# Performance work log

Hardware: AMD Instinct MI355X
Metric: run time of the kernel (lower is better)

The kernel has to match this reference:

```python
import jax, jax.numpy as jnp
import numpy as np

N = 100000        # nodes
E = 3200000       # edges (avg degree 32)
D_IN, D_H, D_OUT = 128, 128, 64
EPS = 1e-5        # BatchNorm eps


def setup_inputs() -> dict:
    key = jax.random.key(0)
    ks = jax.random.split(key, 12)
    s = 0.1
    return {
        "x": jax.random.normal(ks[0], (N, D_IN), jnp.float32),
        "edge_index": jax.random.randint(ks[1], (2, E), 0, N, jnp.int32),
        "W1": jax.random.normal(ks[2], (D_IN, D_H), jnp.float32) * s,
        "b1": jnp.zeros((D_H,), jnp.float32),
        "W2": jax.random.normal(ks[3], (D_H, D_H), jnp.float32) * s,
        "b2": jnp.zeros((D_H,), jnp.float32),
        "W3": jax.random.normal(ks[4], (D_H, D_OUT), jnp.float32) * s,
        "b3": jnp.zeros((D_OUT,), jnp.float32),
        "g1": jnp.ones((D_H,), jnp.float32),
        "be1": jnp.zeros((D_H,), jnp.float32),
        "g2": jnp.ones((D_H,), jnp.float32),
        "be2": jnp.zeros((D_H,), jnp.float32),
    }


def reference(x, edge_index, W1, b1, W2, b2, W3, b3, g1, be1, g2, be2):
    # GCNConv normalization: add self-loops, symmetric deg^-1/2 A deg^-1/2
    loop = jnp.arange(N, dtype=edge_index.dtype)
    src = jnp.concatenate([edge_index[0], loop])   # [E+N]
    dst = jnp.concatenate([edge_index[1], loop])   # [E+N]
    deg = jax.ops.segment_sum(jnp.ones(src.shape, x.dtype), dst, num_segments=N)
    dinv = jnp.where(deg > 0, jax.lax.rsqrt(deg), 0.0)
    norm = (dinv[src] * dinv[dst])[:, None]        # [E+N, 1]

    def conv(h, W, b):
        h = h @ W                                   # dense transform [N, d]
        msg = h[src] * norm                         # gather + scale [E+N, d]
        return jax.ops.segment_sum(msg, dst, num_segments=N) + b

    def bn(h, g, be):  # BatchNorm1d over nodes (batch stats, eval-style dropout)
        m = h.mean(axis=0)
        v = h.var(axis=0)
        return (h - m) * jax.lax.rsqrt(v + EPS) * g + be

    h = jax.nn.relu(bn(conv(x, W1, b1), g1, be1))
    h = jax.nn.relu(bn(conv(h, W2, b2), g2, be2))
    h = conv(h, W3, b3)
    return jax.nn.softmax(h, axis=1)
```

## Files before the change

### kernel.cpp

```cpp
#include <hip/hip_runtime.h>
#include <hip/hip_fp16.h>

constexpr int   NN   = 100000;
constexpr int   NE   = 3200000;
constexpr float BN_EPS = 1e-5f;

constexpr int MG_B  = (NN / 32 + 3) / 4;
constexpr int NB    = (NN + 127) / 128;
constexpr int HB    = 256;
constexpr int CHUNK = NE / HB;
constexpr int BKT_CAP = 5120;
constexpr int IDX_CAP = 1536;
constexpr int NPAN = 8;

typedef _Float16 half8 __attribute__((ext_vector_type(8)));
typedef float    floatx16 __attribute__((ext_vector_type(16)));
typedef float    floatx8  __attribute__((ext_vector_type(8)));
typedef int      intx4   __attribute__((ext_vector_type(4)));


__global__ __launch_bounds__(256) void k_wprep_all(const float* __restrict__ W1,
                                                   const float* __restrict__ W2,
                                                   const float* __restrict__ W3,
                                                   _Float16* __restrict__ Wt1,
                                                   _Float16* __restrict__ Wt2,
                                                   _Float16* __restrict__ Wt3) {
  int idx = blockIdx.x * 256 + threadIdx.x;
  if (idx < 16384) {
    int k = idx >> 7, n = idx & 127;
    Wt1[n * 128 + k] = (_Float16)W1[idx];
  } else if (idx < 32768) {
    int j = idx - 16384, k = j >> 7, n = j & 127;
    Wt2[n * 128 + k] = (_Float16)W2[j];
  } else if (idx < 40960) {
    int j = idx - 32768, k = j >> 6, n = j & 63;
    Wt3[n * 128 + k] = (_Float16)W3[j];
  }
}

__global__ __launch_bounds__(256) void k_f1(const int* __restrict__ dst,
                                            int* __restrict__ blkhist,
                                            const float* __restrict__ x,
                                            const _Float16* __restrict__ Wt1,
                                            _Float16* __restrict__ C) {
  __shared__ int h[NB];
  if (blockIdx.x < MG_B) {
    int wid  = (blockIdx.x * 256 + threadIdx.x) >> 6;
    int lane = threadIdx.x & 63;
    if (wid >= NN / 32) return;
    const int m = lane & 31;
    const int q = lane >> 5;
    const int row0 = wid * 32;
    const float* Arow = x + (size_t)(row0 + m) * 128 + q * 8;

    floatx16 acc[4] = {};
#pragma unroll
    for (int s = 0; s < 8; ++s) {
      float4 a0 = *(const float4*)(Arow + 16 * s);
      float4 a1 = *(const float4*)(Arow + 16 * s + 4);
      half8 af;
      af[0] = (_Float16)a0.x; af[1] = (_Float16)a0.y;
      af[2] = (_Float16)a0.z; af[3] = (_Float16)a0.w;
      af[4] = (_Float16)a1.x; af[5] = (_Float16)a1.y;
      af[6] = (_Float16)a1.z; af[7] = (_Float16)a1.w;
#pragma unroll
      for (int ct = 0; ct < 4; ++ct) {
        half8 bf = *(const half8*)(Wt1 + (size_t)(ct * 32 + m) * 128 + q * 8 + 16 * s);
        acc[ct] = __builtin_amdgcn_mfma_f32_32x32x16_f16(af, bf, acc[ct], 0, 0, 0);
      }
    }
#pragma unroll
    for (int ct = 0; ct < 4; ++ct) {
      int p = ct * 2 + (m >> 4);
      int off = m & 15;
#pragma unroll
      for (int r = 0; r < 16; ++r) {
        int row = (r & 3) + 8 * (r >> 2) + 4 * q;
        C[((size_t)p * NN + row0 + row) * 16 + off] = (_Float16)acc[ct][r];
      }
    }
  } else {
    int j = blockIdx.x - MG_B;
    int t = threadIdx.x;
    for (int b = t; b < NB; b += 256) h[b] = 0;
    __syncthreads();
    int base = j * CHUNK;
    for (int e = base + t; e < base + CHUNK; e += 256)
      atomicAdd(&h[dst[e] >> 7], 1);
    __syncthreads();
    for (int b = t; b < NB; b += 256) blkhist[j * NB + b] = h[b];
  }
}

__global__ __launch_bounds__(256) void k_scan_bkt_a(const int* __restrict__ blkhist,
                                                    int* __restrict__ blkbase,
                                                    int* __restrict__ total) {
  int wid  = (blockIdx.x * 256 + threadIdx.x) >> 6;
  int lane = threadIdx.x & 63;
  if (wid >= NB) return;
  int i0 = lane * 4;
  int v0 = blkhist[(i0 + 0) * NB + wid];
  int v1 = blkhist[(i0 + 1) * NB + wid];
  int v2 = blkhist[(i0 + 2) * NB + wid];
  int v3 = blkhist[(i0 + 3) * NB + wid];
  int lt = v0 + v1 + v2 + v3;
  int inc = lt;
#pragma unroll
  for (int off = 1; off < 64; off <<= 1) {
    int xx = __shfl_up(inc, off);
    if (lane >= off) inc += xx;
  }
  int exc = inc - lt;
  blkbase[(i0 + 0) * NB + wid] = exc;
  blkbase[(i0 + 1) * NB + wid] = exc + v0;
  blkbase[(i0 + 2) * NB + wid] = exc + v0 + v1;
  blkbase[(i0 + 3) * NB + wid] = exc + v0 + v1 + v2;
  if (lane == 63) total[wid] = inc;
}

__global__ __launch_bounds__(1024) void k_scan_bkt_b(const int* __restrict__ total,
                                                     int* __restrict__ bbase) {
  __shared__ int s[1024];
  int t = threadIdx.x;
  int v = (t < NB) ? total[t] : 0;
  s[t] = v;
  __syncthreads();
  for (int off = 1; off < 1024; off <<= 1) {
    int xx = (t >= off) ? s[t - off] : 0;
    __syncthreads();
    s[t] += xx;
    __syncthreads();
  }
  if (t < NB) bbase[t] = s[t] - v;
  if (t == NB - 1) bbase[NB] = s[t];
}

__global__ __launch_bounds__(256) void k_scatter(const int* __restrict__ ei,
                                                 const int* __restrict__ bbase,
                                                 const int* __restrict__ blkbase,
                                                 int* __restrict__ ebuf) {
  __shared__ int cur[NB];
  int i = blockIdx.x;
  int t = threadIdx.x;
  for (int b = t; b < NB; b += 256) cur[b] = bbase[b] + blkbase[i * NB + b];
  __syncthreads();
  int base = i * CHUNK;
  for (int e = base + t; e < base + CHUNK; e += 256) {
    int s = ei[e];
    int d = ei[NE + e];
    int b = d >> 7;
    int pos = atomicAdd(&cur[b], 1);
    ebuf[pos] = s | ((d & 127) << 17);
  }
}

__global__ __launch_bounds__(256) void k_bucket(const int* __restrict__ bbase,
                                                const int* __restrict__ ebuf,
                                                int* __restrict__ rowptr,
                                                float* __restrict__ dinv,
                                                int* __restrict__ csrc,
                                                _Float16* __restrict__ Hf) {
  __shared__ int degL[128];
  __shared__ int sc[128];
  __shared__ int curL[128];
  __shared__ float dvs[128];
  __shared__ int sorted[BKT_CAP];
  int b = blockIdx.x;
  int t = threadIdx.x;
  int e0 = bbase[b], e1 = bbase[b + 1];
  int cnt = e1 - e0;
  if (t < 128) degL[t] = 0;
  __syncthreads();
  for (int e = e0 + t; e < e1; e += 256)
    atomicAdd(&degL[ebuf[e] >> 17], 1);
  __syncthreads();
  if (t < 128) sc[t] = degL[t];
  __syncthreads();
  for (int off = 1; off < 128; off <<= 1) {
    int xx = 0;
    if (t < 128 && t >= off) xx = sc[t - off];
    __syncthreads();
    if (t < 128) sc[t] += xx;
    __syncthreads();
  }
  if (t < 128) {
    int node = b * 128 + t;
    float dv = 0.f;
    if (node < NN) {
      int d = degL[t];
      int exc = sc[t] - d;
      rowptr[node] = e0 + exc;
      dv = rsqrtf((float)(d + 1));
      dinv[node] = dv;
      curL[t] = exc;
    }
    dvs[t] = dv;
  }
  if (b == NB - 1 && t == 0) rowptr[NN] = NE;
  __syncthreads();
  if (cnt <= BKT_CAP) {
    for (int e = e0 + t; e < e1; e += 256) {
      int p = ebuf[e];
      int pos = atomicAdd(&curL[p >> 17], 1);
      sorted[pos] = p & 0x1FFFF;
    }
    __syncthreads();
    for (int i = t; i < cnt; i += 256) csrc[e0 + i] = sorted[i];
  } else {
    for (int e = e0 + t; e < e1; e += 256) {
      int p = ebuf[e];
      int pos = atomicAdd(&curL[p >> 17], 1);
      csrc[e0 + pos] = p & 0x1FFFF;
    }
  }
  int node = b * 128 + (t >> 1);
  if (node < NN) {
    float dv = dvs[t >> 1];
    size_t base = (size_t)node * 16 + (t & 1) * 8;
#pragma unroll
    for (int k = 0; k < NPAN; ++k) {
      size_t a = (size_t)k * (NN * 16) + base;
      half8 h = *(const half8*)(Hf + a);
#pragma unroll
      for (int j = 0; j < 8; ++j) h[j] = (_Float16)((float)h[j] * dv);
      *(half8*)(Hf + a) = h;
    }
  }
}

template <int BN_, bool POUT>
__global__ __launch_bounds__(256) void k_mgemm(const _Float16* __restrict__ A,
                                               const _Float16* __restrict__ Wt,
                                               const float* __restrict__ scale,
                                               const float* __restrict__ shift,
                                               const float* __restrict__ dinv,
                                               _Float16* __restrict__ C) {
  constexpr int NCT = BN_ / 32;
  int wid  = (blockIdx.x * 256 + threadIdx.x) >> 6;
  int lane = threadIdx.x & 63;
  if (wid >= NN / 32) return;
  const int m = lane & 31;
  const int q = lane >> 5;
  const int row0 = wid * 32;

  const _Float16* Abase = A + (size_t)(row0 + m) * 16 + q * 8;

  floatx16 acc[NCT] = {};

#pragma unroll
  for (int s = 0; s < 8; ++s) {
    half8 raw = *(const half8*)(Abase + (size_t)s * (NN * 16));
    int k0 = 16 * s + q * 8;
    half8 af;
#pragma unroll
    for (int j = 0; j < 8; ++j) {
      float a = fmaxf(fmaf((float)raw[j], scale[k0 + j], shift[k0 + j]), 0.f);
      af[j] = (_Float16)a;
    }
#pragma unroll
    for (int ct = 0; ct < NCT; ++ct) {
      half8 bf = *(const half8*)(Wt + (size_t)(ct * 32 + m) * 128 + q * 8 + 16 * s);
      acc[ct] = __builtin_amdgcn_mfma_f32_32x32x16_f16(af, bf, acc[ct], 0, 0, 0);
    }
  }

#pragma unroll
  for (int ct = 0; ct < NCT; ++ct) {
    int p = ct * 2 + (m >> 4);
    int off = m & 15;
#pragma unroll
    for (int r = 0; r < 16; ++r) {
      int row = (r & 3) + 8 * (r >> 2) + 4 * q;
      float dv = dinv[row0 + row];
      _Float16 val = (_Float16)(acc[ct][r] * dv);
      if (POUT)
        C[((size_t)p * NN + row0 + row) * 16 + off] = val;
      else
        C[(size_t)(row0 + row) * BN_ + ct * 32 + m] = val;
    }
  }
}

__global__ __launch_bounds__(256) void k_agg128p(const _Float16* __restrict__ Hp,
                                                 const float* __restrict__ dinv,
                                                 const int* __restrict__ rowptr,
                                                 const int* __restrict__ srcs,
                                                 _Float16* __restrict__ outp) {
  __shared__ int sidx[4][IDX_CAP];
  int p  = blockIdx.x & 7;
  int nb = blockIdx.x >> 3;
  int t  = threadIdx.x;
  int w    = t >> 6;
  int lane = t & 63;
  int pr = lane >> 1;
  int hi = lane & 1;
  int node = nb * 128 + w * 32 + pr;
  int nodec = node < NN ? node : NN - 1;
  int beg = rowptr[nodec];
  int end = rowptr[nodec + 1];
  int w0   = __shfl(beg, 0);
  int wend = __shfl(end, 62);
  int cnt  = wend - w0;
  int* my = sidx[w];
  int scnt = cnt < IDX_CAP ? cnt : IDX_CAP;
  for (int i = lane; i < scnt; i += 64)
    my[i] = __builtin_nontemporal_load(srcs + w0 + i);

  const _Float16* base = Hp + (size_t)p * (NN * 16) + hi * 8;
  floatx8 acc = {};
  if (node < NN) {
    half8 h = *(const half8*)(base + (size_t)node * 16);
#pragma unroll
    for (int j = 0; j < 8; ++j) acc[j] = (float)h[j];
    int lb = beg - w0, le = end - w0;
    int e = lb;
    if (le <= IDX_CAP) {
      for (; e + 4 <= le; e += 4) {
        int s0 = my[e + 0], s1 = my[e + 1], s2 = my[e + 2], s3 = my[e + 3];
        half8 h0 = *(const half8*)(base + (size_t)s0 * 16);
        half8 h1 = *(const half8*)(base + (size_t)s1 * 16);
        half8 h2 = *(const half8*)(base + (size_t)s2 * 16);
        half8 h3 = *(const half8*)(base + (size_t)s3 * 16);
#pragma unroll
        for (int j = 0; j < 8; ++j)
          acc[j] += ((float)h0[j] + (float)h1[j]) + ((float)h2[j] + (float)h3[j]);
      }
      for (; e < le; ++e) {
        half8 h0 = *(const half8*)(base + (size_t)my[e] * 16);
#pragma unroll
        for (int j = 0; j < 8; ++j) acc[j] += (float)h0[j];
      }
    } else {
      for (e = beg; e < end; ++e) {
        half8 h0 = *(const half8*)(base + (size_t)srcs[e] * 16);
#pragma unroll
        for (int j = 0; j < 8; ++j) acc[j] += (float)h0[j];
      }
    }
    float di = dinv[node];
    __half2 o[4];
#pragma unroll
    for (int j = 0; j < 4; ++j)
      o[j] = __floats2half2_rn(acc[2 * j] * di, acc[2 * j + 1] * di);
    intx4* dst = (intx4*)(outp + ((size_t)p * NN + node) * 16 + hi * 8);
    __builtin_nontemporal_store(*(const intx4*)o, dst);
  }
}

__global__ __launch_bounds__(256) void k_agg64_softmax(const __half* __restrict__ H,
                                                       const float* __restrict__ dinv,
                                                       const int* __restrict__ rowptr,
                                                       const int* __restrict__ srcs,
                                                       const float* __restrict__ b3,
                                                       float* __restrict__ out) {
  int wid  = (blockIdx.x * 256 + threadIdx.x) >> 6;
  int lane = threadIdx.x & 63;
  if (wid >= NN) return;
  const int g  = lane >> 3;
  const int sl = lane & 7;
  const _Float16* Hb = (const _Float16*)H + (size_t)sl * 8;
  floatx8 acc = {};
  if (g == 0) {
    half8 h = *(const half8*)(Hb + (size_t)wid * 64);
#pragma unroll
    for (int j = 0; j < 8; ++j) acc[j] = (float)h[j];
  }
  int beg = rowptr[wid], end = rowptr[wid + 1];
  int n = end - beg;
  int chunk = (n + 7) >> 3;
  int e  = beg + g * chunk; if (e > end) e = end;
  int ce = e + chunk;       if (ce > end) ce = end;
  for (; e + 4 <= ce; e += 4) {
    int s0 = srcs[e + 0], s1 = srcs[e + 1];
    int s2 = srcs[e + 2], s3 = srcs[e + 3];
    half8 h0 = *(const half8*)(Hb + (size_t)s0 * 64);
    half8 h1 = *(const half8*)(Hb + (size_t)s1 * 64);
    half8 h2 = *(const half8*)(Hb + (size_t)s2 * 64);
    half8 h3 = *(const half8*)(Hb + (size_t)s3 * 64);
#pragma unroll
    for (int j = 0; j < 8; ++j)
      acc[j] += ((float)h0[j] + (float)h1[j]) + ((float)h2[j] + (float)h3[j]);
  }
  for (; e < ce; ++e) {
    half8 h0 = *(const half8*)(Hb + (size_t)srcs[e] * 64);
#pragma unroll
    for (int j = 0; j < 8; ++j) acc[j] += (float)h0[j];
  }
#pragma unroll
  for (int j = 0; j < 8; ++j) {
    acc[j] += __shfl_xor(acc[j], 8);
    acc[j] += __shfl_xor(acc[j], 16);
    acc[j] += __shfl_xor(acc[j], 32);
  }
  float di = dinv[wid];
  float4 bA = *(const float4*)(b3 + sl * 8);
  float4 bB = *(const float4*)(b3 + sl * 8 + 4);
  float v[8];
  v[0] = acc[0] * di + bA.x; v[1] = acc[1] * di + bA.y;
  v[2] = acc[2] * di + bA.z; v[3] = acc[3] * di + bA.w;
  v[4] = acc[4] * di + bB.x; v[5] = acc[5] * di + bB.y;
  v[6] = acc[6] * di + bB.z; v[7] = acc[7] * di + bB.w;
  float m = v[0];
#pragma unroll
  for (int j = 1; j < 8; ++j) m = fmaxf(m, v[j]);
  m = fmaxf(m, __shfl_xor(m, 1));
  m = fmaxf(m, __shfl_xor(m, 2));
  m = fmaxf(m, __shfl_xor(m, 4));
  float s = 0.f;
#pragma unroll
  for (int j = 0; j < 8; ++j) { v[j] = __expf(v[j] - m); s += v[j]; }
  s += __shfl_xor(s, 1);
  s += __shfl_xor(s, 2);
  s += __shfl_xor(s, 4);
  float inv = 1.0f / s;
  if (g == 0) {
    float4 oA = {v[0] * inv, v[1] * inv, v[2] * inv, v[3] * inv};
    float4 oB = {v[4] * inv, v[5] * inv, v[6] * inv, v[7] * inv};
    *(float4*)(out + (size_t)wid * 64 + sl * 8)     = oA;
    *(float4*)(out + (size_t)wid * 64 + sl * 8 + 4) = oB;
  }
}

__global__ __launch_bounds__(256) void k_stats(const __half2* __restrict__ H2,
                                               float* __restrict__ S1,
                                               float* __restrict__ S2) {
  int t = threadIdx.x;
  int cp = t & 63;
  int r = t >> 6;
  const __half2* Pb = H2 + (size_t)(cp >> 3) * (NN * 8) + (cp & 7);
  float2 s1 = {0.f, 0.f}, s2 = {0.f, 0.f};
  for (int row = blockIdx.x * 4 + r; row < NN; row += gridDim.x * 4) {
    float2 v = __half22float2(Pb[(size_t)row * 8]);
    s1.x += v.x; s1.y += v.y;
    s2.x += v.x * v.x; s2.y += v.y * v.y;
  }
  __shared__ float2 l1[256], l2[256];
  l1[t] = s1; l2[t] = s2;
  __syncthreads();
  if (t < 128) {
    l1[t].x += l1[t+128].x; l1[t].y += l1[t+128].y;
    l2[t].x += l2[t+128].x; l2[t].y += l2[t+128].y;
  }
  __syncthreads();
  if (t < 64) {
    float2 a1 = l1[t], b1 = l1[t+64];
    float2 a2 = l2[t], b2 = l2[t+64];
    atomicAdd(&S1[2*cp+0], a1.x + b1.x);
    atomicAdd(&S1[2*cp+1], a1.y + b1.y);
    atomicAdd(&S2[2*cp+0], a2.x + b2.x);
    atomicAdd(&S2[2*cp+1], a2.y + b2.y);
  }
}

__global__ void k_finalize(const float* __restrict__ S1, const float* __restrict__ S2,
                           const float* __restrict__ g,  const float* __restrict__ be,
                           float* __restrict__ scale,    float* __restrict__ shift) {
  int t = threadIdx.x;
  float mean = S1[t] * (1.0f / NN);
  float var  = S2[t] * (1.0f / NN) - mean * mean;
  float is   = rsqrtf(var + BN_EPS);
  float sc   = g[t] * is;
  scale[t] = sc;
  shift[t] = be[t] - mean * sc;
}

extern "C" void kernel_launch(void* const* d_in, const int* in_sizes, int n_in,
                              void* d_out, int out_size, void* d_ws, size_t ws_size,
                              hipStream_t stream) {
  (void)in_sizes; (void)n_in; (void)out_size; (void)ws_size;
  const float* x   = (const float*)d_in[0];
  const int*   ei  = (const int*)d_in[1];
  const float* W1  = (const float*)d_in[2];
  const float* W2  = (const float*)d_in[4];
  const float* W3  = (const float*)d_in[6];
  const float* b3  = (const float*)d_in[7];
  const float* g1  = (const float*)d_in[8];
  const float* be1 = (const float*)d_in[9];
  const float* g2  = (const float*)d_in[10];
  const float* be2 = (const float*)d_in[11];
  float* out = (float*)d_out;

  char* ws = (char*)d_ws;
  size_t off = 0;
  auto take = [&](size_t bytes) -> char* {
    char* p = ws + off;
    off = (off + bytes + 255) & ~(size_t)255;
    return p;
  };
  float* S1a    = (float*)take(128 * 4);
  float* S2a    = (float*)take(128 * 4);
  float* S1b    = (float*)take(128 * 4);
  float* S2b    = (float*)take(128 * 4);
  size_t zero_bytes = off;
  float* scale1 = (float*)take(128 * 4);
  float* shift1 = (float*)take(128 * 4);
  float* scale2 = (float*)take(128 * 4);
  float* shift2 = (float*)take(128 * 4);
  float* dinv   = (float*)take((size_t)NN * 4);
  int*   rowptr = (int*)  take((size_t)(NN + 1) * 4);
  int*   bbase  = (int*)  take((size_t)(NB + 1) * 4);
  int*   total  = (int*)  take((size_t)NB * 4);
  int*   blkhist= (int*)  take((size_t)HB * NB * 4);
  int*   blkbase= (int*)  take((size_t)HB * NB * 4);
  int*   ebuf   = (int*)  take((size_t)NE * 4);
  int*   csrc   = (int*)  take((size_t)NE * 4);
  _Float16* Wt1 = (_Float16*)take((size_t)128 * 128 * 2);
  _Float16* Wt2 = (_Float16*)take((size_t)128 * 128 * 2);
  _Float16* Wt3 = (_Float16*)take((size_t)64 * 128 * 2);
  _Float16* Hf  = (_Float16*)take((size_t)NN * 128 * 2);
  _Float16* hB  = (_Float16*)take((size_t)NN * 128 * 2);

  (void)hipMemsetAsync(d_ws, 0, zero_bytes, stream);

  const int mgB  = MG_B;
  const int aggB = (NN + 3) / 4;
  const int aggPB = NPAN * ((NN + 127) / 128);
  const int scanAB = (NB + 3) / 4;

  k_wprep_all<<<160, 256, 0, stream>>>(W1, W2, W3, Wt1, Wt2, Wt3);

  k_f1<<<MG_B + HB, 256, 0, stream>>>(ei + NE, blkhist, x, Wt1, Hf);

  k_scan_bkt_a<<<scanAB, 256, 0, stream>>>(blkhist, blkbase, total);
  k_scan_bkt_b<<<1, 1024, 0, stream>>>(total, bbase);
  k_scatter<<<HB, 256, 0, stream>>>(ei, bbase, blkbase, ebuf);
  k_bucket<<<NB, 256, 0, stream>>>(bbase, ebuf, rowptr, dinv, csrc, Hf);

  k_agg128p<<<aggPB, 256, 0, stream>>>(Hf, dinv, rowptr, csrc, hB);
  k_stats<<<1024, 256, 0, stream>>>((const __half2*)hB, S1a, S2a);
  k_finalize<<<1, 128, 0, stream>>>(S1a, S2a, g1, be1, scale1, shift1);

  k_mgemm<128, true><<<mgB, 256, 0, stream>>>(hB, Wt2, scale1, shift1, dinv, Hf);
  k_agg128p<<<aggPB, 256, 0, stream>>>(Hf, dinv, rowptr, csrc, hB);
  k_stats<<<1024, 256, 0, stream>>>((const __half2*)hB, S1b, S2b);
  k_finalize<<<1, 128, 0, stream>>>(S1b, S2b, g2, be2, scale2, shift2);

  k_mgemm<64, false><<<mgB, 256, 0, stream>>>(hB, Wt3, scale2, shift2, dinv, Hf);
  k_agg64_softmax<<<aggB, 256, 0, stream>>>((const __half*)Hf, dinv, rowptr, csrc, b3, out);
}
```

Measured before the change: 789.5 us.

## Split each node's neighbor gather across eight lane slots in panel aggregation

The 128-wide panel aggregation kernel moves from one node per lane pair to four nodes per wave, with eight slots per node that each take a strided share of the edges (self-loop folded in as item zero), and combines partial sums with xor shuffles. This spreads the gathers for one node over more lanes, so more independent loads are in flight per wave and load imbalance between high- and low-degree nodes inside a wave is reduced. In exchange the grid grows eightfold, there are shuffle reductions and a block barrier, the shared index buffer is smaller with a global fallback, and the output store is no longer nontemporal. Some offset expressions are also widened to size_t.

Measured after the change: 729.4 us. 1.08x faster.

```diff
diff --git a/kernel.cpp b/kernel.cpp
--- a/kernel.cpp
+++ b/kernel.cpp
@@ -10,7 +10,7 @@
 constexpr int HB    = 256;
 constexpr int CHUNK = NE / HB;
 constexpr int BKT_CAP = 5120;
-constexpr int IDX_CAP = 1536;
+constexpr int IDXW = 512;
 constexpr int NPAN = 8;
 
 typedef _Float16 half8 __attribute__((ext_vector_type(8)));
@@ -219,7 +219,7 @@
     size_t base = (size_t)node * 16 + (t & 1) * 8;
 #pragma unroll
     for (int k = 0; k < NPAN; ++k) {
-      size_t a = (size_t)k * (NN * 16) + base;
+      size_t a = (size_t)k * ((size_t)NN * 16) + base;
       half8 h = *(const half8*)(Hf + a);
 #pragma unroll
       for (int j = 0; j < 8; ++j) h[j] = (_Float16)((float)h[j] * dv);
@@ -249,7 +249,7 @@
 
 #pragma unroll
   for (int s = 0; s < 8; ++s) {
-    half8 raw = *(const half8*)(Abase + (size_t)s * (NN * 16));
+    half8 raw = *(const half8*)(Abase + (size_t)s * ((size_t)NN * 16));
     int k0 = 16 * s + q * 8;
     half8 af;
 #pragma unroll
@@ -286,64 +286,82 @@
                                                  const int* __restrict__ rowptr,
                                                  const int* __restrict__ srcs,
                                                  _Float16* __restrict__ outp) {
-  __shared__ int sidx[4][IDX_CAP];
+  __shared__ int sidx[4][IDXW];
   int p  = blockIdx.x & 7;
   int nb = blockIdx.x >> 3;
   int t  = threadIdx.x;
   int w    = t >> 6;
   int lane = t & 63;
-  int pr = lane >> 1;
-  int hi = lane & 1;
-  int node = nb * 128 + w * 32 + pr;
-  int nodec = node < NN ? node : NN - 1;
-  int beg = rowptr[nodec];
-  int end = rowptr[nodec + 1];
+  int nid  = lane >> 4;
+  int slot = (lane >> 1) & 7;
+  int half = lane & 1;
+  int node = nb * 16 + w * 4 + nid;
+
+  int beg = rowptr[node];
+  int end = rowptr[node + 1];
   int w0   = __shfl(beg, 0);
-  int wend = __shfl(end, 62);
+  int wend = __shfl(end, 63);
   int cnt  = wend - w0;
   int* my = sidx[w];
-  int scnt = cnt < IDX_CAP ? cnt : IDX_CAP;
-  for (int i = lane; i < scnt; i += 64)
-    my[i] = __builtin_nontemporal_load(srcs + w0 + i);
-
-  const _Float16* base = Hp + (size_t)p * (NN * 16) + hi * 8;
+  bool fits = (cnt <= IDXW);
+  if (fits)
+    for (int i = lane; i < cnt; i += 64) my[i] = srcs[w0 + i];
+  __syncthreads();
+
+  int items = end - beg + 1;
+  int nit = (items + 7) >> 3;
+  int mx = nit;
+  mx = max(mx, __shfl_xor(mx, 16));
+  mx = max(mx, __shfl_xor(mx, 32));
+
+  const _Float16* base = Hp + (size_t)p * ((size_t)NN * 16) + half * 8;
+  int lo = beg - w0;
   floatx8 acc = {};
-  if (node < NN) {
-    half8 h = *(const half8*)(base + (size_t)node * 16);
-#pragma unroll
-    for (int j = 0; j < 8; ++j) acc[j] = (float)h[j];
-    int lb = beg - w0, le = end - w0;
-    int e = lb;
-    if (le <= IDX_CAP) {
-      for (; e + 4 <= le; e += 4) {
-        int s0 = my[e + 0], s1 = my[e + 1], s2 = my[e + 2], s3 = my[e + 3];
-        half8 h0 = *(const half8*)(base + (size_t)s0 * 16);
-        half8 h1 = *(const half8*)(base + (size_t)s1 * 16);
-        half8 h2 = *(const half8*)(base + (size_t)s2 * 16);
-        half8 h3 = *(const half8*)(base + (size_t)s3 * 16);
-#pragma unroll
-        for (int j = 0; j < 8; ++j)
-          acc[j] += ((float)h0[j] + (float)h1[j]) + ((float)h2[j] + (float)h3[j]);
-      }
-      for (; e < le; ++e) {
-        half8 h0 = *(const half8*)(base + (size_t)my[e] * 16);
-#pragma unroll
-        for (int j = 0; j < 8; ++j) acc[j] += (float)h0[j];
-      }
-    } else {
-      for (e = beg; e < end; ++e) {
-        half8 h0 = *(const half8*)(base + (size_t)srcs[e] * 16);
-#pragma unroll
-        for (int j = 0; j < 8; ++j) acc[j] += (float)h0[j];
-      }
-    }
+
+  int it = 0;
+  for (; it + 2 <= mx; it += 2) {
+    int j0 = it * 8 + slot;
+    int j1 = j0 + 8;
+    bool v0 = j0 < items;
+    bool v1 = j1 < items;
+    int r0 = node, r1 = node;
+    if (v0 && j0 > 0) r0 = fits ? my[lo + j0 - 1] : srcs[beg + j0 - 1];
+    if (v1)           r1 = fits ? my[lo + j1 - 1] : srcs[beg + j1 - 1];
+    if (v0) {
+      half8 h0 = *(const half8*)(base + (size_t)r0 * 16);
+#pragma unroll
+      for (int k = 0; k < 8; ++k) acc[k] += (float)h0[k];
+    }
+    if (v1) {
+      half8 h1 = *(const half8*)(base + (size_t)r1 * 16);
+#pragma unroll
+      for (int k = 0; k < 8; ++k) acc[k] += (float)h1[k];
+    }
+  }
+  for (; it < mx; ++it) {
+    int j0 = it * 8 + slot;
+    if (j0 < items) {
+      int r0 = node;
+      if (j0 > 0) r0 = fits ? my[lo + j0 - 1] : srcs[beg + j0 - 1];
+      half8 h0 = *(const half8*)(base + (size_t)r0 * 16);
+#pragma unroll
+      for (int k = 0; k < 8; ++k) acc[k] += (float)h0[k];
+    }
+  }
+
+#pragma unroll
+  for (int k = 0; k < 8; ++k) {
+    acc[k] += __shfl_xor(acc[k], 2);
+    acc[k] += __shfl_xor(acc[k], 4);
+    acc[k] += __shfl_xor(acc[k], 8);
+  }
+  if (slot == 0) {
     float di = dinv[node];
     __half2 o[4];
 #pragma unroll
     for (int j = 0; j < 4; ++j)
       o[j] = __floats2half2_rn(acc[2 * j] * di, acc[2 * j + 1] * di);
-    intx4* dst = (intx4*)(outp + ((size_t)p * NN + node) * 16 + hi * 8);
-    __builtin_nontemporal_store(*(const intx4*)o, dst);
+    *(intx4*)(outp + ((size_t)p * NN + node) * 16 + half * 8) = *(const intx4*)o;
   }
 }
 
@@ -427,7 +445,7 @@
   int t = threadIdx.x;
   int cp = t & 63;
   int r = t >> 6;
-  const __half2* Pb = H2 + (size_t)(cp >> 3) * (NN * 8) + (cp & 7);
+  const __half2* Pb = H2 + (size_t)(cp >> 3) * ((size_t)NN * 8) + (cp & 7);
   float2 s1 = {0.f, 0.f}, s2 = {0.f, 0.f};
   for (int row = blockIdx.x * 4 + r; row < NN; row += gridDim.x * 4) {
     float2 v = __half22float2(Pb[(size_t)row * 8]);
@@ -514,7 +532,7 @@
 
   const int mgB  = MG_B;
   const int aggB = (NN + 3) / 4;
-  const int aggPB = NPAN * ((NN + 127) / 128);
+  const int aggPB = NPAN * (NN / 16);
   const int scanAB = (NB + 3) / 4;
 
   k_wprep_all<<<160, 256, 0, stream>>>(W1, W2, W3, Wt1, Wt2, Wt3);
```
